# Kernel tuning notes

Hardware: AMD Instinct MI355X
Metric: run time of the kernel (lower is better)

Reference implementation:

```python
import jax, jax.numpy as jnp
import numpy as np

E = 600_000
NUM_RADIAL = 6
HIDDEN = 128
OUT = 256
NUM_LAYERS = 3
N_NODES = 50_000


def setup_inputs() -> dict:
    key = jax.random.key(0)
    ks = jax.random.split(key, 6)
    x = jax.random.normal(ks[0], (E, HIDDEN), dtype=jnp.float32)
    rbf = jax.random.normal(ks[1], (E, NUM_RADIAL), dtype=jnp.float32)
    i = jax.random.randint(ks[2], (E,), 0, N_NODES, dtype=jnp.int64)
    # Linear weights stored as [in, out] so y = x @ W (equivalent to torch x @ W.T)
    W_rbf = jax.random.normal(ks[3], (NUM_RADIAL, HIDDEN), dtype=jnp.float32) / np.sqrt(NUM_RADIAL)
    W_down = jax.random.normal(ks[4], (HIDDEN, OUT), dtype=jnp.float32) / np.sqrt(HIDDEN)
    Ws = jax.random.normal(ks[5], (NUM_LAYERS, OUT, OUT), dtype=jnp.float32) / np.sqrt(OUT)
    bs = jnp.zeros((NUM_LAYERS, OUT), dtype=jnp.float32)
    return {"x": x, "rbf": rbf, "i": i, "W_rbf": W_rbf, "W_down": W_down,
            "Ws": Ws, "bs": bs, "num_nodes": N_NODES}


def reference(x, rbf, i, W_rbf, W_down, Ws, bs, num_nodes):
    # elementwise gate: lin_rbf(rbf) * x  -> [E, hidden]
    g = (rbf @ W_rbf) * x
    # scatter-add over edge target index i -> [num_nodes, hidden]
    h = jax.ops.segment_sum(g, i, num_segments=num_nodes)
    # down projection -> [num_nodes, out]
    h = h @ W_down
    # dense MLP stack with SiLU
    for k in range(Ws.shape[0]):
        h = jax.nn.silu(h @ Ws[k] + bs[k])
    return h
```

## Files before the change

### kernel.cpp

```cpp
#include <hip/hip_runtime.h>
#include <hip/hip_bf16.h>
#include <cstdint>

typedef __attribute__((ext_vector_type(8))) short short8;
typedef __attribute__((ext_vector_type(4))) float floatx4;

#define HIDDEN 128
#define NOUT 256

__global__ __launch_bounds__(256) void prep_weights(
    const float* __restrict__ Wd, const float* __restrict__ Ws,
    __hip_bfloat16* __restrict__ WdT, __hip_bfloat16* __restrict__ WsT)
{
    int tid = blockIdx.x * 256 + threadIdx.x;
    if (tid < 256 * 128) {
        int n = tid >> 7, k = tid & 127;
        WdT[tid] = __float2bfloat16(Wd[k * 256 + n]);
    }
    int tid2 = tid - 256 * 128;
    if (tid2 >= 0 && tid2 < 3 * 256 * 256) {
        int l = tid2 >> 16;
        int rem = tid2 & 65535;
        int n = rem >> 8, k = rem & 255;
        WsT[tid2] = __float2bfloat16(Ws[l * 65536 + k * 256 + n]);
    }
}

__global__ __launch_bounds__(256) void hist_k(
    const int* __restrict__ idx, int* __restrict__ cnt, int E)
{
    int e = blockIdx.x * 256 + threadIdx.x;
    if (e < E) atomicAdd(&cnt[idx[e]], 1);
}

__global__ __launch_bounds__(1024) void exscan_k(
    const int* __restrict__ cnt, int* __restrict__ offsets,
    int* __restrict__ cursor, int M)
{
    __shared__ int lds[1024];
    __shared__ int carry_s;
    int t = threadIdx.x;
    if (t == 0) carry_s = 0;
    __syncthreads();
    for (int base = 0; base < M; base += 1024) {
        int v = (base + t < M) ? cnt[base + t] : 0;
        lds[t] = v;
        __syncthreads();
        for (int s = 1; s < 1024; s <<= 1) {
            int a = (t >= s) ? lds[t - s] : 0;
            __syncthreads();
            lds[t] += a;
            __syncthreads();
        }
        int incl = lds[t];
        int c = carry_s;
        __syncthreads();
        if (t == 1023) carry_s = c + incl;
        if (base + t < M) {
            int ex = c + incl - v;
            offsets[base + t] = ex;
            cursor[base + t] = ex;
        }
        __syncthreads();
    }
    if (t == 0) offsets[M] = carry_s;
}

__global__ __launch_bounds__(256) void fill_k(
    const int* __restrict__ idx, int* __restrict__ cursor,
    int* __restrict__ edge_ids, int E)
{
    int e = blockIdx.x * 256 + threadIdx.x;
    if (e < E) {
        int pos = atomicAdd(&cursor[idx[e]], 1);
        edge_ids[pos] = e;
    }
}

__global__ __launch_bounds__(256) void gather_k(
    const float* __restrict__ x, const float* __restrict__ rbf,
    const float* __restrict__ Wrbf, const int* __restrict__ offsets,
    const int* __restrict__ edge_ids, float* __restrict__ hacc, int M)
{
    int t = threadIdx.x;
    int wave = t >> 6, lane = t & 63;
    int n = blockIdx.x * 4 + wave;
    if (n >= M) return;

    int c0 = lane * 2;
    float w0[6], w1[6];
#pragma unroll
    for (int r = 0; r < 6; ++r) {
        w0[r] = Wrbf[r * HIDDEN + c0];
        w1[r] = Wrbf[r * HIDDEN + c0 + 1];
    }

    int s = offsets[n], eend = offsets[n + 1];
    float a0 = 0.f, a1 = 0.f;
    for (int p = s; p < eend; ++p) {
        int e = __builtin_amdgcn_readfirstlane(edge_ids[p]);
        const float* rb = &rbf[(long)e * 6];
        float p0 = 0.f, p1 = 0.f;
#pragma unroll
        for (int r = 0; r < 6; ++r) {
            float rv = rb[r];
            p0 += rv * w0[r];
            p1 += rv * w1[r];
        }
        float2 xv = *(const float2*)&x[(long)e * HIDDEN + c0];
        a0 += p0 * xv.x;
        a1 += p1 * xv.y;
    }
    *(float2*)&hacc[(long)n * HIDDEN + c0] = make_float2(a0, a1);
}

template <int K, bool A_F32, bool BIAS, bool SILU, bool OUT_F32>
__global__ __launch_bounds__(256) void gemm_k(
    const void* __restrict__ Ap, const __hip_bfloat16* __restrict__ BT,
    const float* __restrict__ bias, void* __restrict__ Cp, int M)
{
    __shared__ __hip_bfloat16 Al[64][72];
    __shared__ __hip_bfloat16 Bl[256][72];

    int t = threadIdx.x;
    int lane = t & 63, w = t >> 6;
    int q = lane >> 4, r16 = lane & 15;
    int m0 = blockIdx.x * 64;

    floatx4 acc[4][4] = {};

    for (int k0 = 0; k0 < K; k0 += 64) {
        if (A_F32) {
            const float* A = (const float*)Ap;
#pragma unroll
            for (int it = 0; it < 4; ++it) {
                int idx = it * 256 + t;
                int row = idx >> 4;
                int col = (idx & 15) * 4;
                int gr = m0 + row; if (gr >= M) gr = M - 1;
                float4 v = *(const float4*)&A[(long)gr * K + k0 + col];
                Al[row][col + 0] = __float2bfloat16(v.x);
                Al[row][col + 1] = __float2bfloat16(v.y);
                Al[row][col + 2] = __float2bfloat16(v.z);
                Al[row][col + 3] = __float2bfloat16(v.w);
            }
        } else {
            const __hip_bfloat16* A = (const __hip_bfloat16*)Ap;
#pragma unroll
            for (int it = 0; it < 2; ++it) {
                int idx = it * 256 + t;
                int row = idx >> 3;
                int col = (idx & 7) * 8;
                int gr = m0 + row; if (gr >= M) gr = M - 1;
                uint4 v = *(const uint4*)&A[(long)gr * K + k0 + col];
                *(uint4*)&Al[row][col] = v;
            }
        }
#pragma unroll
        for (int it = 0; it < 8; ++it) {
            int idx = it * 256 + t;
            int row = idx >> 3;
            int col = (idx & 7) * 8;
            uint4 v = *(const uint4*)&BT[(long)row * K + k0 + col];
            *(uint4*)&Bl[row][col] = v;
        }
        __syncthreads();

#pragma unroll
        for (int kt = 0; kt < 2; ++kt) {
            short8 af[4], bfr[4];
#pragma unroll
            for (int mt = 0; mt < 4; ++mt)
                af[mt] = *(const short8*)&Al[mt * 16 + r16][kt * 32 + q * 8];
#pragma unroll
            for (int nt = 0; nt < 4; ++nt)
                bfr[nt] = *(const short8*)&Bl[w * 64 + nt * 16 + r16][kt * 32 + q * 8];
#pragma unroll
            for (int mt = 0; mt < 4; ++mt)
#pragma unroll
                for (int nt = 0; nt < 4; ++nt)
                    acc[mt][nt] = __builtin_amdgcn_mfma_f32_16x16x32_bf16(
                        af[mt], bfr[nt], acc[mt][nt], 0, 0, 0);
        }
        __syncthreads();
    }

#pragma unroll
    for (int mt = 0; mt < 4; ++mt) {
#pragma unroll
        for (int rr = 0; rr < 4; ++rr) {
            int row = m0 + mt * 16 + q * 4 + rr;
            if (row < M) {
#pragma unroll
                for (int nt = 0; nt < 4; ++nt) {
                    int col = w * 64 + nt * 16 + r16;
                    float v = acc[mt][nt][rr];
                    if (BIAS) v += bias[col];
                    if (SILU) v = v / (1.f + __expf(-v));
                    if (OUT_F32)
                        ((float*)Cp)[(long)row * NOUT + col] = v;
                    else
                        ((__hip_bfloat16*)Cp)[(long)row * NOUT + col] = __float2bfloat16(v);
                }
            }
        }
    }
}

extern "C" void kernel_launch(void* const* d_in, const int* in_sizes, int n_in,
                              void* d_out, int out_size, void* d_ws, size_t ws_size,
                              hipStream_t stream)
{
    const float* x    = (const float*)d_in[0];
    const float* rbf  = (const float*)d_in[1];
    const int*   idx  = (const int*)d_in[2];
    const float* Wrbf = (const float*)d_in[3];
    const float* Wd   = (const float*)d_in[4];
    const float* Ws   = (const float*)d_in[5];
    const float* bs   = (const float*)d_in[6];

    int E = in_sizes[0] / HIDDEN;
    int M = out_size / NOUT;

    char* ws = (char*)d_ws;
    float* hacc = (float*)ws;
    size_t off = (size_t)M * HIDDEN * sizeof(float);
    __hip_bfloat16* actA = (__hip_bfloat16*)(ws + off); off += (size_t)M * NOUT * 2;
    __hip_bfloat16* actB = (__hip_bfloat16*)(ws + off); off += (size_t)M * NOUT * 2;
    __hip_bfloat16* WdT  = (__hip_bfloat16*)(ws + off); off += 256 * 128 * 2;
    __hip_bfloat16* WsT  = (__hip_bfloat16*)(ws + off); off += 3 * 256 * 256 * 2;

    char* csr = (char*)actB;
    int* cnt      = (int*)csr;                   csr += (size_t)M * 4;
    int* offsets  = (int*)csr;                   csr += (size_t)(M + 1) * 4;
    int* cursor   = (int*)csr;                   csr += (size_t)M * 4;
    int* edge_ids = (int*)csr;

    hipMemsetAsync(cnt, 0, (size_t)M * sizeof(int), stream);
    prep_weights<<<(256 * 128 + 3 * 256 * 256 + 255) / 256, 256, 0, stream>>>(Wd, Ws, WdT, WsT);
    hist_k<<<(E + 255) / 256, 256, 0, stream>>>(idx, cnt, E);
    exscan_k<<<1, 1024, 0, stream>>>(cnt, offsets, cursor, M);
    fill_k<<<(E + 255) / 256, 256, 0, stream>>>(idx, cursor, edge_ids, E);
    gather_k<<<(M + 3) / 4, 256, 0, stream>>>(x, rbf, Wrbf, offsets, edge_ids, hacc, M);

    int gblocks = (M + 63) / 64;
    gemm_k<128, true,  false, false, false><<<gblocks, 256, 0, stream>>>(hacc, WdT, nullptr, actA, M);
    gemm_k<256, false, true,  true,  false><<<gblocks, 256, 0, stream>>>(actA, WsT,             bs,       actB, M);
    gemm_k<256, false, true,  true,  false><<<gblocks, 256, 0, stream>>>(actB, WsT + 65536,     bs + 256, actA, M);
    gemm_k<256, false, true,  true,  true ><<<gblocks, 256, 0, stream>>>(actA, WsT + 2 * 65536, bs + 512, d_out, M);
}
```

Baseline: 720.7 us.

## Fuse MLP layers into one kernel and parallelize CSR offset scan

Replaces the four separate GEMM launches with one kernel that keeps each 64-row activation tile in LDS across the down projection and all three MLP layers, so intermediate bf16 activations never go through global memory. The single-block serial exclusive scan becomes a three-stage multi-block scan: per-block sums, a one-wave scan of those sums, then per-block offsets. This removes a serial bottleneck of many barriers over 50K nodes. The cost is a larger LDS footprint per block (about 70KB), which can lower occupancy in the fused GEMM, and two extra small launches for the scan.

```diff
diff --git a/kernel.cpp b/kernel.cpp
--- a/kernel.cpp
+++ b/kernel.cpp
@@ -33,37 +33,77 @@
     if (e < E) atomicAdd(&cnt[idx[e]], 1);
 }
 
-__global__ __launch_bounds__(1024) void exscan_k(
-    const int* __restrict__ cnt, int* __restrict__ offsets,
-    int* __restrict__ cursor, int M)
-{
-    __shared__ int lds[1024];
-    __shared__ int carry_s;
+__global__ __launch_bounds__(256) void scan_blocksum_k(
+    const int* __restrict__ cnt, int* __restrict__ blocksum, int M)
+{
+    int base = blockIdx.x * 1024;
     int t = threadIdx.x;
-    if (t == 0) carry_s = 0;
+    int s = 0;
+#pragma unroll
+    for (int j = 0; j < 4; ++j) {
+        int p = base + t * 4 + j;
+        if (p < M) s += cnt[p];
+    }
+#pragma unroll
+    for (int d = 32; d > 0; d >>= 1) s += __shfl_down(s, d);
+    __shared__ int wsum[4];
+    if ((t & 63) == 0) wsum[t >> 6] = s;
     __syncthreads();
-    for (int base = 0; base < M; base += 1024) {
-        int v = (base + t < M) ? cnt[base + t] : 0;
-        lds[t] = v;
-        __syncthreads();
-        for (int s = 1; s < 1024; s <<= 1) {
-            int a = (t >= s) ? lds[t - s] : 0;
-            __syncthreads();
-            lds[t] += a;
-            __syncthreads();
-        }
-        int incl = lds[t];
-        int c = carry_s;
-        __syncthreads();
-        if (t == 1023) carry_s = c + incl;
-        if (base + t < M) {
-            int ex = c + incl - v;
-            offsets[base + t] = ex;
-            cursor[base + t] = ex;
-        }
-        __syncthreads();
-    }
-    if (t == 0) offsets[M] = carry_s;
+    if (t == 0) blocksum[blockIdx.x] = wsum[0] + wsum[1] + wsum[2] + wsum[3];
+}
+
+__global__ __launch_bounds__(64) void scan_base_k(
+    const int* __restrict__ blocksum, int* __restrict__ blockbase,
+    int* __restrict__ offsets, int nb, int M)
+{
+    int lane = threadIdx.x;
+    int carry = 0;
+    for (int base = 0; base < nb; base += 64) {
+        int v = (base + lane < nb) ? blocksum[base + lane] : 0;
+        int incl = v;
+#pragma unroll
+        for (int d = 1; d < 64; d <<= 1) {
+            int u = __shfl_up(incl, d);
+            if (lane >= d) incl += u;
+        }
+        if (base + lane < nb) blockbase[base + lane] = carry + incl - v;
+        carry += __shfl(incl, 63);
+    }
+    if (lane == 0) offsets[M] = carry;
+}
+
+__global__ __launch_bounds__(256) void scan_offsets_k(
+    const int* __restrict__ cnt, const int* __restrict__ blockbase,
+    int* __restrict__ offsets, int* __restrict__ cursor, int M)
+{
+    int base = blockIdx.x * 1024;
+    int t = threadIdx.x, lane = t & 63, wv = t >> 6;
+    int v[4];
+    int s = 0;
+#pragma unroll
+    for (int j = 0; j < 4; ++j) {
+        int p = base + t * 4 + j;
+        v[j] = (p < M) ? cnt[p] : 0;
+        s += v[j];
+    }
+    int incl = s;
+#pragma unroll
+    for (int d = 1; d < 64; d <<= 1) {
+        int u = __shfl_up(incl, d);
+        if (lane >= d) incl += u;
+    }
+    __shared__ int wtot[4];
+    if (lane == 63) wtot[wv] = incl;
+    __syncthreads();
+    int wbase = 0;
+    for (int j = 0; j < wv; ++j) wbase += wtot[j];
+    int start = blockbase[blockIdx.x] + wbase + incl - s;
+#pragma unroll
+    for (int j = 0; j < 4; ++j) {
+        int p = base + t * 4 + j;
+        if (p < M) { offsets[p] = start; cursor[p] = start; }
+        start += v[j];
+    }
 }
 
 __global__ __launch_bounds__(256) void fill_k(
@@ -114,93 +154,99 @@
     *(float2*)&hacc[(long)n * HIDDEN + c0] = make_float2(a0, a1);
 }
 
-template <int K, bool A_F32, bool BIAS, bool SILU, bool OUT_F32>
-__global__ __launch_bounds__(256) void gemm_k(
-    const void* __restrict__ Ap, const __hip_bfloat16* __restrict__ BT,
-    const float* __restrict__ bias, void* __restrict__ Cp, int M)
-{
-    __shared__ __hip_bfloat16 Al[64][72];
-    __shared__ __hip_bfloat16 Bl[256][72];
+__global__ __launch_bounds__(256) void mlp_fused(
+    const float* __restrict__ hacc, const __hip_bfloat16* __restrict__ WdT,
+    const __hip_bfloat16* __restrict__ WsT, const float* __restrict__ bs,
+    float* __restrict__ out, int M)
+{
+    __shared__ __hip_bfloat16 Al[64][264];
+    __shared__ __hip_bfloat16 Wl[256][72];
 
     int t = threadIdx.x;
     int lane = t & 63, w = t >> 6;
     int q = lane >> 4, r16 = lane & 15;
     int m0 = blockIdx.x * 64;
 
-    floatx4 acc[4][4] = {};
-
-    for (int k0 = 0; k0 < K; k0 += 64) {
-        if (A_F32) {
-            const float* A = (const float*)Ap;
-#pragma unroll
-            for (int it = 0; it < 4; ++it) {
-                int idx = it * 256 + t;
-                int row = idx >> 4;
-                int col = (idx & 15) * 4;
-                int gr = m0 + row; if (gr >= M) gr = M - 1;
-                float4 v = *(const float4*)&A[(long)gr * K + k0 + col];
-                Al[row][col + 0] = __float2bfloat16(v.x);
-                Al[row][col + 1] = __float2bfloat16(v.y);
-                Al[row][col + 2] = __float2bfloat16(v.z);
-                Al[row][col + 3] = __float2bfloat16(v.w);
-            }
-        } else {
-            const __hip_bfloat16* A = (const __hip_bfloat16*)Ap;
-#pragma unroll
-            for (int it = 0; it < 2; ++it) {
+#pragma unroll
+    for (int it = 0; it < 8; ++it) {
+        int idx = it * 256 + t;
+        int row = idx >> 5;
+        int col = (idx & 31) * 4;
+        int gr = m0 + row; if (gr >= M) gr = M - 1;
+        float4 v = *(const float4*)&hacc[(long)gr * HIDDEN + col];
+        Al[row][col + 0] = __float2bfloat16(v.x);
+        Al[row][col + 1] = __float2bfloat16(v.y);
+        Al[row][col + 2] = __float2bfloat16(v.z);
+        Al[row][col + 3] = __float2bfloat16(v.w);
+    }
+    __syncthreads();
+
+    for (int layer = 0; layer < 4; ++layer) {
+        const int K = (layer == 0) ? 128 : 256;
+        const __hip_bfloat16* BT = (layer == 0) ? WdT : WsT + (layer - 1) * 65536;
+        floatx4 acc[4][4] = {};
+
+        for (int k0 = 0; k0 < K; k0 += 64) {
+#pragma unroll
+            for (int it = 0; it < 8; ++it) {
                 int idx = it * 256 + t;
                 int row = idx >> 3;
                 int col = (idx & 7) * 8;
-                int gr = m0 + row; if (gr >= M) gr = M - 1;
-                uint4 v = *(const uint4*)&A[(long)gr * K + k0 + col];
-                *(uint4*)&Al[row][col] = v;
-            }
-        }
-#pragma unroll
-        for (int it = 0; it < 8; ++it) {
-            int idx = it * 256 + t;
-            int row = idx >> 3;
-            int col = (idx & 7) * 8;
-            uint4 v = *(const uint4*)&BT[(long)row * K + k0 + col];
-            *(uint4*)&Bl[row][col] = v;
-        }
-        __syncthreads();
-
-#pragma unroll
-        for (int kt = 0; kt < 2; ++kt) {
-            short8 af[4], bfr[4];
-#pragma unroll
-            for (int mt = 0; mt < 4; ++mt)
-                af[mt] = *(const short8*)&Al[mt * 16 + r16][kt * 32 + q * 8];
-#pragma unroll
-            for (int nt = 0; nt < 4; ++nt)
-                bfr[nt] = *(const short8*)&Bl[w * 64 + nt * 16 + r16][kt * 32 + q * 8];
-#pragma unroll
-            for (int mt = 0; mt < 4; ++mt)
+                *(uint4*)&Wl[row][col] = *(const uint4*)&BT[(long)row * K + k0 + col];
+            }
+            __syncthreads();
+#pragma unroll
+            for (int kt = 0; kt < 2; ++kt) {
+                short8 af[4], bfr[4];
+#pragma unroll
+                for (int mt = 0; mt < 4; ++mt)
+                    af[mt] = *(const short8*)&Al[mt * 16 + r16][k0 + kt * 32 + q * 8];
 #pragma unroll
                 for (int nt = 0; nt < 4; ++nt)
-                    acc[mt][nt] = __builtin_amdgcn_mfma_f32_16x16x32_bf16(
-                        af[mt], bfr[nt], acc[mt][nt], 0, 0, 0);
-        }
-        __syncthreads();
-    }
-
-#pragma unroll
-    for (int mt = 0; mt < 4; ++mt) {
-#pragma unroll
-        for (int rr = 0; rr < 4; ++rr) {
-            int row = m0 + mt * 16 + q * 4 + rr;
-            if (row < M) {
-#pragma unroll
-                for (int nt = 0; nt < 4; ++nt) {
-                    int col = w * 64 + nt * 16 + r16;
-                    float v = acc[mt][nt][rr];
-                    if (BIAS) v += bias[col];
-                    if (SILU) v = v / (1.f + __expf(-v));
-                    if (OUT_F32)
-                        ((float*)Cp)[(long)row * NOUT + col] = v;
-                    else
-                        ((__hip_bfloat16*)Cp)[(long)row * NOUT + col] = __float2bfloat16(v);
+                    bfr[nt] = *(const short8*)&Wl[w * 64 + nt * 16 + r16][kt * 32 + q * 8];
+#pragma unroll
+                for (int mt = 0; mt < 4; ++mt)
+#pragma unroll
+                    for (int nt = 0; nt < 4; ++nt)
+                        acc[mt][nt] = __builtin_amdgcn_mfma_f32_16x16x32_bf16(
+                            af[mt], bfr[nt], acc[mt][nt], 0, 0, 0);
+            }
+            __syncthreads();
+        }
+
+        if (layer < 3) {
+            const float* bias = (layer == 0) ? nullptr : bs + (layer - 1) * 256;
+#pragma unroll
+            for (int mt = 0; mt < 4; ++mt) {
+#pragma unroll
+                for (int rr = 0; rr < 4; ++rr) {
+                    int row = mt * 16 + q * 4 + rr;
+#pragma unroll
+                    for (int nt = 0; nt < 4; ++nt) {
+                        int col = w * 64 + nt * 16 + r16;
+                        float v = acc[mt][nt][rr];
+                        if (layer > 0) { v += bias[col]; v = v / (1.f + __expf(-v)); }
+                        Al[row][col] = __float2bfloat16(v);
+                    }
+                }
+            }
+            __syncthreads();
+        } else {
+            const float* bias = bs + 2 * 256;
+#pragma unroll
+            for (int mt = 0; mt < 4; ++mt) {
+#pragma unroll
+                for (int rr = 0; rr < 4; ++rr) {
+                    int row = m0 + mt * 16 + q * 4 + rr;
+                    if (row < M) {
+#pragma unroll
+                        for (int nt = 0; nt < 4; ++nt) {
+                            int col = w * 64 + nt * 16 + r16;
+                            float v = acc[mt][nt][rr] + bias[col];
+                            v = v / (1.f + __expf(-v));
+                            out[(long)row * NOUT + col] = v;
+                        }
+                    }
                 }
             }
         }
@@ -221,31 +267,27 @@
 
     int E = in_sizes[0] / HIDDEN;
     int M = out_size / NOUT;
+    int nb = (M + 1023) / 1024;
 
     char* ws = (char*)d_ws;
     float* hacc = (float*)ws;
     size_t off = (size_t)M * HIDDEN * sizeof(float);
-    __hip_bfloat16* actA = (__hip_bfloat16*)(ws + off); off += (size_t)M * NOUT * 2;
-    __hip_bfloat16* actB = (__hip_bfloat16*)(ws + off); off += (size_t)M * NOUT * 2;
-    __hip_bfloat16* WdT  = (__hip_bfloat16*)(ws + off); off += 256 * 128 * 2;
-    __hip_bfloat16* WsT  = (__hip_bfloat16*)(ws + off); off += 3 * 256 * 256 * 2;
-
-    char* csr = (char*)actB;
-    int* cnt      = (int*)csr;                   csr += (size_t)M * 4;
-    int* offsets  = (int*)csr;                   csr += (size_t)(M + 1) * 4;
-    int* cursor   = (int*)csr;                   csr += (size_t)M * 4;
-    int* edge_ids = (int*)csr;
+    __hip_bfloat16* WdT = (__hip_bfloat16*)(ws + off); off += 256 * 128 * 2;
+    __hip_bfloat16* WsT = (__hip_bfloat16*)(ws + off); off += 3 * 256 * 256 * 2;
+    int* cnt       = (int*)(ws + off); off += (size_t)M * 4;
+    int* offsets   = (int*)(ws + off); off += (size_t)(M + 1) * 4;
+    int* cursor    = (int*)(ws + off); off += (size_t)M * 4;
+    int* edge_ids  = (int*)(ws + off); off += (size_t)E * 4;
+    int* blocksum  = (int*)(ws + off); off += (size_t)nb * 4;
+    int* blockbase = (int*)(ws + off); off += (size_t)nb * 4;
 
     hipMemsetAsync(cnt, 0, (size_t)M * sizeof(int), stream);
     prep_weights<<<(256 * 128 + 3 * 256 * 256 + 255) / 256, 256, 0, stream>>>(Wd, Ws, WdT, WsT);
     hist_k<<<(E + 255) / 256, 256, 0, stream>>>(idx, cnt, E);
-    exscan_k<<<1, 1024, 0, stream>>>(cnt, offsets, cursor, M);
+    scan_blocksum_k<<<nb, 256, 0, stream>>>(cnt, blocksum, M);
+    scan_base_k<<<1, 64, 0, stream>>>(blocksum, blockbase, offsets, nb, M);
+    scan_offsets_k<<<nb, 256, 0, stream>>>(cnt, blockbase, offsets, cursor, M);
     fill_k<<<(E + 255) / 256, 256, 0, stream>>>(idx, cursor, edge_ids, E);
     gather_k<<<(M + 3) / 4, 256, 0, stream>>>(x, rbf, Wrbf, offsets, edge_ids, hacc, M);
-
-    int gblocks = (M + 63) / 64;
-    gemm_k<128, true,  false, false, false><<<gblocks, 256, 0, stream>>>(hacc, WdT, nullptr, actA, M);
-    gemm_k<256, false, true,  true,  false><<<gblocks, 256, 0, stream>>>(actA, WsT,             bs,       actB, M);
-    gemm_k<256, false, true,  true,  false><<<gblocks, 256, 0, stream>>>(actB, WsT + 65536,     bs + 256, actA, M);
-    gemm_k<256, false, true,  true,  true ><<<gblocks, 256, 0, stream>>>(actA, WsT + 2 * 65536, bs + 512, d_out, M);
-}
+    mlp_fused<<<(M + 63) / 64, 256, 0, stream>>>(hacc, WdT, WsT, bs, (float*)d_out, M);
+}
```

Measured after the change: 709.7 us. No clear change (-1.5%).
